# Kernel optimization log

Measured on AMD Instinct MI355X. Metric: run time of the kernel, lower is better.

The kernel has to match this reference:

```python
import jax, jax.numpy as jnp
import numpy as np

M_DIM = 1024
N_HEADS = 16
H_DIM = M_DIM // N_HEADS
FFN_H = 2 * M_DIM
B, S = 2, 2048
EPS = 1e-5
NEG = -1e9


def layernorm(x, g, b):
    mu = jnp.mean(x, axis=-1, keepdims=True)
    var = jnp.mean((x - mu) ** 2, axis=-1, keepdims=True)
    return (x - mu) * jax.lax.rsqrt(var + EPS) * g + b


def setup_inputs() -> dict:
    key = jax.random.key(0)
    ks = jax.random.split(key, 16)
    sc = 0.02
    return {
        "x": jax.random.normal(ks[0], (B, S, M_DIM), jnp.float32),
        "attention_mask": jnp.ones((B, S), jnp.int32),
        # per-head QKV projections stacked over heads: [H, M, D]
        "Wq": jax.random.normal(ks[1], (N_HEADS, M_DIM, H_DIM), jnp.float32) * sc,
        "bq": jnp.zeros((N_HEADS, H_DIM), jnp.float32),
        "Wk": jax.random.normal(ks[2], (N_HEADS, M_DIM, H_DIM), jnp.float32) * sc,
        "bk": jnp.zeros((N_HEADS, H_DIM), jnp.float32),
        "Wv": jax.random.normal(ks[3], (N_HEADS, M_DIM, H_DIM), jnp.float32) * sc,
        "bv": jnp.zeros((N_HEADS, H_DIM), jnp.float32),
        "Wo": jax.random.normal(ks[4], (M_DIM, M_DIM), jnp.float32) * sc,
        "bo": jnp.zeros((M_DIM,), jnp.float32),
        "g1": jnp.ones((M_DIM,), jnp.float32),
        "b1": jnp.zeros((M_DIM,), jnp.float32),
        "W1": jax.random.normal(ks[5], (M_DIM, FFN_H), jnp.float32) * sc,
        "bias1": jnp.zeros((FFN_H,), jnp.float32),
        "W2": jax.random.normal(ks[6], (FFN_H, M_DIM), jnp.float32) * sc,
        "bias2": jnp.zeros((M_DIM,), jnp.float32),
        "g2": jnp.ones((M_DIM,), jnp.float32),
        "b2": jnp.zeros((M_DIM,), jnp.float32),
    }


def reference(x, attention_mask, Wq, bq, Wk, bk, Wv, bv, Wo, bo, g1, b1, W1, bias1, W2, bias2, g2, b2):
    # All heads at once (the torch code loops over heads; same math).
    q = jnp.einsum("bsm,hmd->bhsd", x, Wq) + bq[None, :, None, :]
    k = jnp.einsum("bsm,hmd->bhsd", x, Wk) + bk[None, :, None, :]
    v = jnp.einsum("bsm,hmd->bhsd", x, Wv) + bv[None, :, None, :]
    scores = jnp.einsum("bhqd,bhkd->bhqk", q, k) / jnp.sqrt(jnp.float32(H_DIM))
    mask = attention_mask[:, None, None, :].astype(bool)  # [B,1,1,S] over keys
    scores = jnp.where(mask, scores, NEG)
    attn = jax.nn.softmax(scores, axis=-1)
    ctx = jnp.einsum("bhqk,bhkd->bhqd", attn, v)
    ctx = ctx.transpose(0, 2, 1, 3).reshape(x.shape[0], x.shape[1], M_DIM)  # concat heads
    out = ctx @ Wo + bo
    out = layernorm(out + x, g1, b1)
    fout = jax.nn.relu(out @ W1 + bias1) @ W2 + bias2
    out = layernorm(out + fout, g2, b2)
    return out
```

## Files before the change

kernel.cpp:

```cpp
#include <hip/hip_runtime.h>

#define MDIM 1024
#define FFH  2048
#define SEQ  2048
#define AST  72
#define VST  136
#define QSCL 0.18033688f

#if __has_builtin(__builtin_amdgcn_exp2f)
  #define EXP2(x) __builtin_amdgcn_exp2f(x)
#else
  #define EXP2(x) exp2f(x)
#endif

typedef __attribute__((ext_vector_type(8))) __bf16 bf16x8;
typedef __attribute__((ext_vector_type(4))) float floatx4;
typedef __attribute__((address_space(3))) unsigned int lds_uint;
typedef const __attribute__((address_space(1))) unsigned int g_uint;

__device__ __forceinline__ unsigned short f2bf(float f){
  union { float f; unsigned u; } v; v.f = f;
  unsigned u = v.u;
  u += 0x7fffu + ((u >> 16) & 1u);
  return (unsigned short)(u >> 16);
}
__device__ __forceinline__ unsigned short f2bf_tr(float f){
  union { float f; unsigned u; } v; v.f = f;
  return (unsigned short)(v.u >> 16);
}

__global__ void k_cvt_qb(const float* __restrict__ x, unsigned short* __restrict__ xb,
                         const float* __restrict__ bq, const float* __restrict__ bk,
                         const float* __restrict__ bv, float* __restrict__ qbias){
  const int bid = blockIdx.x, t = threadIdx.x;
  if (bid < 4096){
    int i = (bid * 256 + t) * 4;
    float4 v = *(const float4*)(x + i);
    ushort4 o;
    o.x = f2bf(v.x); o.y = f2bf(v.y); o.z = f2bf(v.z); o.w = f2bf(v.w);
    *(ushort4*)(xb + i) = o;
  } else {
    int i = (bid - 4096) * 256 + t;
    qbias[i] = (i < 1024) ? bq[i] * QSCL : (i < 2048) ? bk[i - 1024] : bv[i - 2048];
  }
}

__global__ void __launch_bounds__(256) k_prep_w(const float* __restrict__ Wo, const float* __restrict__ W1,
                                                const float* __restrict__ W2, const float* __restrict__ Wq,
                                                const float* __restrict__ Wk, const float* __restrict__ Wv,
                                                unsigned short* __restrict__ wot, unsigned short* __restrict__ w1t,
                                                unsigned short* __restrict__ w2t, unsigned short* __restrict__ wqkvt){
  __shared__ unsigned short Ts[32 * 36];
  const int t = threadIdx.x, bid = blockIdx.x;
  const int lr = t >> 3, lc4 = (t & 7) << 2;
  if (bid >= 5120){
    const int id = bid - 5120;
    const int xm = id & 31, yd = (id >> 5) & 1, z = id >> 6;
    const int tensor = z >> 4, h = z & 15;
    const float* W = (tensor == 0) ? Wq : (tensor == 1) ? Wk : Wv;
    const float scl = (tensor == 0) ? QSCL : 1.0f;
    const int m0 = xm << 5, d0 = yd << 5;
    float4 v = *(const float4*)(W + ((size_t)h << 16) + (size_t)(m0 + lr) * 64 + d0 + lc4);
    ushort4 o; o.x = f2bf(v.x * scl); o.y = f2bf(v.y * scl); o.z = f2bf(v.z * scl); o.w = f2bf(v.w * scl);
    *(ushort4*)&Ts[lr * 36 + lc4] = o;
    __syncthreads();
    ushort4 w;
    w.x = Ts[(lc4 + 0) * 36 + lr];
    w.y = Ts[(lc4 + 1) * 36 + lr];
    w.z = Ts[(lc4 + 2) * 36 + lr];
    w.w = Ts[(lc4 + 3) * 36 + lr];
    const int n = (tensor << 10) + (h << 6) + d0 + lr;
    *(ushort4*)(wqkvt + ((size_t)n << 10) + m0 + lc4) = w;
    return;
  }
  const float* src; unsigned short* dst; int K, N, k0, n0;
  if (bid < 1024){
    src = Wo; dst = wot; K = 1024; N = 1024;
    n0 = (bid & 31) << 5; k0 = (bid >> 5) << 5;
  } else if (bid < 3072){
    const int id = bid - 1024;
    src = W1; dst = w1t; K = 1024; N = 2048;
    n0 = (id & 63) << 5; k0 = (id >> 6) << 5;
  } else {
    const int id = bid - 3072;
    src = W2; dst = w2t; K = 2048; N = 1024;
    n0 = (id & 31) << 5; k0 = (id >> 5) << 5;
  }
  float4 v = *(const float4*)(src + (size_t)(k0 + lr) * N + n0 + lc4);
  ushort4 o; o.x = f2bf(v.x); o.y = f2bf(v.y); o.z = f2bf(v.z); o.w = f2bf(v.w);
  *(ushort4*)&Ts[lr * 36 + lc4] = o;
  __syncthreads();
  ushort4 w;
  w.x = Ts[(lc4 + 0) * 36 + lr];
  w.y = Ts[(lc4 + 1) * 36 + lr];
  w.z = Ts[(lc4 + 2) * 36 + lr];
  w.w = Ts[(lc4 + 3) * 36 + lr];
  *(ushort4*)(dst + (size_t)(n0 + lr) * K + k0 + lc4) = w;
}

template<int RELU, int OUTBF>
__global__ void __launch_bounds__(256) k_gemm128(const unsigned short* __restrict__ A,
                                                 const unsigned short* __restrict__ Bt,
                                                 const float* __restrict__ bias,
                                                 void* __restrict__ Cout, int N, int K){
  __shared__ unsigned short As[2 * 128 * 32];
  __shared__ unsigned short Bs[2 * 128 * 32];
  const int t = threadIdx.x;
  const int m0 = blockIdx.y << 7, n0 = blockIdx.x << 7;
  const int lane = t & 63, w = t >> 6;
  const int quad = lane >> 4, l16 = lane & 15;
  const int mw = (w & 1) << 6, nw = (w >> 1) << 6;
  floatx4 acc[4][4];
  #pragma unroll
  for (int i = 0; i < 4; i++)
    #pragma unroll
    for (int j = 0; j < 4; j++) acc[i][j] = (floatx4){0.f, 0.f, 0.f, 0.f};
  const unsigned short* Ag  = A  + (size_t)(m0 + (t >> 2)) * K + ((t & 3) << 3);
  const unsigned short* Ag2 = Ag + (size_t)64 * K;
  const unsigned short* Bg  = Bt + (size_t)(n0 + (t >> 2)) * K + ((t & 3) << 3);
  const unsigned short* Bg2 = Bg + (size_t)64 * K;
  for (int kb = 0; kb < K; kb += 64){
    #pragma unroll
    for (int s = 0; s < 2; s++){
      const int ko = kb + (s << 5), lo = (s << 12) + (t << 3);
      __builtin_amdgcn_global_load_lds((g_uint*)(Ag  + ko), (lds_uint*)&As[lo],        16, 0, 0);
      __builtin_amdgcn_global_load_lds((g_uint*)(Ag2 + ko), (lds_uint*)&As[lo + 2048], 16, 0, 0);
      __builtin_amdgcn_global_load_lds((g_uint*)(Bg  + ko), (lds_uint*)&Bs[lo],        16, 0, 0);
      __builtin_amdgcn_global_load_lds((g_uint*)(Bg2 + ko), (lds_uint*)&Bs[lo + 2048], 16, 0, 0);
    }
    __syncthreads();
    #pragma unroll
    for (int s = 0; s < 2; s++){
      const int sb = s << 12;
      bf16x8 af[4], bf[4];
      #pragma unroll
      for (int mt = 0; mt < 4; mt++)
        af[mt] = *(const bf16x8*)&As[sb + ((mw + (mt << 4) + l16) << 5) + (quad << 3)];
      #pragma unroll
      for (int nt = 0; nt < 4; nt++)
        bf[nt] = *(const bf16x8*)&Bs[sb + ((nw + (nt << 4) + l16) << 5) + (quad << 3)];
      #pragma unroll
      for (int mt = 0; mt < 4; mt++)
        #pragma unroll
        for (int nt = 0; nt < 4; nt++)
          acc[mt][nt] = __builtin_amdgcn_mfma_f32_16x16x32_bf16(af[mt], bf[nt], acc[mt][nt], 0, 0, 0);
    }
    __syncthreads();
  }
  #pragma unroll
  for (int nt = 0; nt < 4; nt++){
    const int col = n0 + nw + (nt << 4) + l16;
    const float bsv = bias[col];
    #pragma unroll
    for (int mt = 0; mt < 4; mt++){
      const int row = m0 + mw + (mt << 4) + (quad << 2);
      #pragma unroll
      for (int r = 0; r < 4; r++){
        float v = acc[mt][nt][r] + bsv;
        if (RELU) v = fmaxf(v, 0.f);
        if (OUTBF) ((unsigned short*)Cout)[(size_t)(row + r) * N + col] = f2bf(v);
        else       ((float*)Cout)[(size_t)(row + r) * N + col] = v;
      }
    }
  }
}

template<int RELU, int OUTBF>
__global__ void __launch_bounds__(256) k_gemm64n(const unsigned short* __restrict__ A,
                                                 const unsigned short* __restrict__ Bt,
                                                 const float* __restrict__ bias,
                                                 void* __restrict__ Cout, int N, int K){
  __shared__ unsigned short As[2 * 128 * 32];
  __shared__ unsigned short Bs[2 * 64 * 32];
  const int t = threadIdx.x;
  const int m0 = blockIdx.y << 7, n0 = blockIdx.x << 6;
  const int lane = t & 63, w = t >> 6;
  const int quad = lane >> 4, l16 = lane & 15;
  const int mw = (w & 1) << 6, nw = (w >> 1) << 5;
  floatx4 acc[4][2];
  #pragma unroll
  for (int i = 0; i < 4; i++)
    #pragma unroll
    for (int j = 0; j < 2; j++) acc[i][j] = (floatx4){0.f, 0.f, 0.f, 0.f};
  const unsigned short* Ag  = A  + (size_t)(m0 + (t >> 2)) * K + ((t & 3) << 3);
  const unsigned short* Ag2 = Ag + (size_t)64 * K;
  const unsigned short* Bg  = Bt + (size_t)(n0 + (t >> 2)) * K + ((t & 3) << 3);
  for (int kb = 0; kb < K; kb += 64){
    #pragma unroll
    for (int s = 0; s < 2; s++){
      const int ko = kb + (s << 5);
      __builtin_amdgcn_global_load_lds((g_uint*)(Ag  + ko), (lds_uint*)&As[(s << 12) + (t << 3)],        16, 0, 0);
      __builtin_amdgcn_global_load_lds((g_uint*)(Ag2 + ko), (lds_uint*)&As[(s << 12) + (t << 3) + 2048], 16, 0, 0);
      __builtin_amdgcn_global_load_lds((g_uint*)(Bg  + ko), (lds_uint*)&Bs[(s << 11) + (t << 3)],        16, 0, 0);
    }
    __syncthreads();
    #pragma unroll
    for (int s = 0; s < 2; s++){
      bf16x8 af[4], bf[2];
      #pragma unroll
      for (int mt = 0; mt < 4; mt++)
        af[mt] = *(const bf16x8*)&As[(s << 12) + ((mw + (mt << 4) + l16) << 5) + (quad << 3)];
      #pragma unroll
      for (int nt = 0; nt < 2; nt++)
        bf[nt] = *(const bf16x8*)&Bs[(s << 11) + ((nw + (nt << 4) + l16) << 5) + (quad << 3)];
      #pragma unroll
      for (int mt = 0; mt < 4; mt++)
        #pragma unroll
        for (int nt = 0; nt < 2; nt++)
          acc[mt][nt] = __builtin_amdgcn_mfma_f32_16x16x32_bf16(af[mt], bf[nt], acc[mt][nt], 0, 0, 0);
    }
    __syncthreads();
  }
  #pragma unroll
  for (int nt = 0; nt < 2; nt++){
    const int col = n0 + nw + (nt << 4) + l16;
    const float bsv = bias[col];
    #pragma unroll
    for (int mt = 0; mt < 4; mt++){
      const int row = m0 + mw + (mt << 4) + (quad << 2);
      #pragma unroll
      for (int r = 0; r < 4; r++){
        float v = acc[mt][nt][r] + bsv;
        if (RELU) v = fmaxf(v, 0.f);
        if (OUTBF) ((unsigned short*)Cout)[(size_t)(row + r) * N + col] = f2bf(v);
        else       ((float*)Cout)[(size_t)(row + r) * N + col] = v;
      }
    }
  }
}

__global__ void __launch_bounds__(256, 2) k_attn(const unsigned short* __restrict__ qkvb,
                                                 const int* __restrict__ amask,
                                                 unsigned short* __restrict__ ctxb){
  __shared__ __align__(16) unsigned short Ks[128 * AST];
  __shared__ __align__(16) unsigned short Vt[64 * VST];
  __shared__ __align__(16) unsigned short PQs[128 * VST];
  __shared__ int msk[128];
  const int t = threadIdx.x;
  const int w = t >> 6, lane = t & 63;
  const int quad = lane >> 4, l16 = lane & 15;
  const int b = blockIdx.y >> 4, h = blockIdx.y & 15;
  const int q0 = blockIdx.x << 7;
  const int r0 = (w << 5) + l16;
  const int r1 = r0 + 16;
  const int sr = t >> 2, sc = (t & 3) << 4;
  const int kg = t >> 4, dc = (t & 15) << 2;

  {
    const unsigned short* qs = qkvb + (size_t)((b << 11) + q0 + (t >> 1)) * 3072 + (h << 6) + ((t & 1) << 5);
    unsigned short* qd = &PQs[(t >> 1) * VST + ((t & 1) << 5)];
    *(uint4*)(qd)      = *(const uint4*)(qs);
    *(uint4*)(qd + 8)  = *(const uint4*)(qs + 8);
    *(uint4*)(qd + 16) = *(const uint4*)(qs + 16);
    *(uint4*)(qd + 24) = *(const uint4*)(qs + 24);
  }
  __syncthreads();
  const bf16x8 qa0 = *(const bf16x8*)&PQs[r0 * VST + (quad << 3)];
  const bf16x8 qa1 = *(const bf16x8*)&PQs[r0 * VST + (quad << 3) + 32];
  const bf16x8 qb0 = *(const bf16x8*)&PQs[r1 * VST + (quad << 3)];
  const bf16x8 qb1 = *(const bf16x8*)&PQs[r1 * VST + (quad << 3) + 32];

  floatx4 accA[4], accB[4];
  #pragma unroll
  for (int i = 0; i < 4; i++){
    accA[i] = (floatx4){0.f, 0.f, 0.f, 0.f};
    accB[i] = (floatx4){0.f, 0.f, 0.f, 0.f};
  }
  float l_runA = 0.f, l_runB = 0.f;

  const unsigned short* kbase  = qkvb + (size_t)((b << 11) + sr) * 3072 + 1024 + (h << 6) + sc;
  const unsigned short* kbase2 = kbase + (size_t)64 * 3072;
  const unsigned short* vbase  = qkvb + (size_t)((b << 11) + (kg << 2)) * 3072 + 2048 + (h << 6) + dc;
  const unsigned short* vbase2 = vbase + (size_t)64 * 3072;
  const int* mbase = amask + (b << 11);

  uint4 krA, krB, krC, krD;
  ushort4 va0, va1, va2, va3, vb0, vb1, vb2, vb3;
  int mreg = 1;
  {
    krA = *(const uint4*)kbase;
    krB = *(const uint4*)(kbase + 8);
    krC = *(const uint4*)kbase2;
    krD = *(const uint4*)(kbase2 + 8);
    va0 = *(const ushort4*)(vbase);
    va1 = *(const ushort4*)(vbase + 3072);
    va2 = *(const ushort4*)(vbase + 2 * 3072);
    va3 = *(const ushort4*)(vbase + 3 * 3072);
    vb0 = *(const ushort4*)(vbase2);
    vb1 = *(const ushort4*)(vbase2 + 3072);
    vb2 = *(const ushort4*)(vbase2 + 2 * 3072);
    vb3 = *(const ushort4*)(vbase2 + 3 * 3072);
    if (t < 128) mreg = mbase[t];
  }

  for (int k0 = 0; k0 < SEQ; k0 += 128){
    __syncthreads();
    *(uint4*)&Ks[sr * AST + sc]            = krA;
    *(uint4*)&Ks[sr * AST + sc + 8]        = krB;
    *(uint4*)&Ks[(sr + 64) * AST + sc]     = krC;
    *(uint4*)&Ks[(sr + 64) * AST + sc + 8] = krD;
    {
      ushort4 c;
      c.x = va0.x; c.y = va1.x; c.z = va2.x; c.w = va3.x; *(ushort4*)&Vt[(dc + 0) * VST + (kg << 2)] = c;
      c.x = va0.y; c.y = va1.y; c.z = va2.y; c.w = va3.y; *(ushort4*)&Vt[(dc + 1) * VST + (kg << 2)] = c;
      c.x = va0.z; c.y = va1.z; c.z = va2.z; c.w = va3.z; *(ushort4*)&Vt[(dc + 2) * VST + (kg << 2)] = c;
      c.x = va0.w; c.y = va1.w; c.z = va2.w; c.w = va3.w; *(ushort4*)&Vt[(dc + 3) * VST + (kg << 2)] = c;
      c.x = vb0.x; c.y = vb1.x; c.z = vb2.x; c.w = vb3.x; *(ushort4*)&Vt[(dc + 0) * VST + ((kg + 16) << 2)] = c;
      c.x = vb0.y; c.y = vb1.y; c.z = vb2.y; c.w = vb3.y; *(ushort4*)&Vt[(dc + 1) * VST + ((kg + 16) << 2)] = c;
      c.x = vb0.z; c.y = vb1.z; c.z = vb2.z; c.w = vb3.z; *(ushort4*)&Vt[(dc + 2) * VST + ((kg + 16) << 2)] = c;
      c.x = vb0.w; c.y = vb1.w; c.z = vb2.w; c.w = vb3.w; *(ushort4*)&Vt[(dc + 3) * VST + ((kg + 16) << 2)] = c;
    }
    if (t < 128) msk[t] = mreg;
    __syncthreads();
    if (k0 + 128 < SEQ){
      const unsigned short* ks  = kbase  + (size_t)(k0 + 128) * 3072;
      const unsigned short* ks2 = kbase2 + (size_t)(k0 + 128) * 3072;
      krA = *(const uint4*)ks;
      krB = *(const uint4*)(ks + 8);
      krC = *(const uint4*)ks2;
      krD = *(const uint4*)(ks2 + 8);
      const unsigned short* vs  = vbase  + (size_t)(k0 + 128) * 3072;
      const unsigned short* vs2 = vbase2 + (size_t)(k0 + 128) * 3072;
      va0 = *(const ushort4*)(vs);
      va1 = *(const ushort4*)(vs + 3072);
      va2 = *(const ushort4*)(vs + 2 * 3072);
      va3 = *(const ushort4*)(vs + 3 * 3072);
      vb0 = *(const ushort4*)(vs2);
      vb1 = *(const ushort4*)(vs2 + 3072);
      vb2 = *(const ushort4*)(vs2 + 2 * 3072);
      vb3 = *(const ushort4*)(vs2 + 3 * 3072);
      if (t < 128) mreg = mbase[k0 + 128 + t];
    }

    float lsA = 0.f, lsB = 0.f;
    #pragma unroll
    for (int mt = 0; mt < 8; mt++){
      const unsigned short* kp = &Ks[((mt << 4) + l16) * AST + (quad << 3)];
      const bf16x8 kf0 = *(const bf16x8*)(kp);
      const bf16x8 kf1 = *(const bf16x8*)(kp + 32);
      floatx4 sA = (floatx4){0.f, 0.f, 0.f, 0.f};
      floatx4 sB = (floatx4){0.f, 0.f, 0.f, 0.f};
      __builtin_amdgcn_s_setprio(1);
      sA = __builtin_amdgcn_mfma_f32_16x16x32_bf16(kf0, qa0, sA, 0, 0, 0);
      sA = __builtin_amdgcn_mfma_f32_16x16x32_bf16(kf1, qa1, sA, 0, 0, 0);
      sB = __builtin_amdgcn_mfma_f32_16x16x32_bf16(kf0, qb0, sB, 0, 0, 0);
      sB = __builtin_amdgcn_mfma_f32_16x16x32_bf16(kf1, qb1, sB, 0, 0, 0);
      __builtin_amdgcn_s_setprio(0);
      const int4 m4 = *(const int4*)&msk[(mt << 4) + (quad << 2)];
      float pA0 = m4.x ? EXP2(sA[0]) : 0.f;
      float pA1 = m4.y ? EXP2(sA[1]) : 0.f;
      float pA2 = m4.z ? EXP2(sA[2]) : 0.f;
      float pA3 = m4.w ? EXP2(sA[3]) : 0.f;
      lsA += pA0 + pA1 + pA2 + pA3;
      ushort4 oA;
      oA.x = f2bf_tr(pA0); oA.y = f2bf_tr(pA1); oA.z = f2bf_tr(pA2); oA.w = f2bf_tr(pA3);
      *(ushort4*)&PQs[r0 * VST + (mt << 4) + (quad << 2)] = oA;
      float pB0 = m4.x ? EXP2(sB[0]) : 0.f;
      float pB1 = m4.y ? EXP2(sB[1]) : 0.f;
      float pB2 = m4.z ? EXP2(sB[2]) : 0.f;
      float pB3 = m4.w ? EXP2(sB[3]) : 0.f;
      lsB += pB0 + pB1 + pB2 + pB3;
      ushort4 oB;
      oB.x = f2bf_tr(pB0); oB.y = f2bf_tr(pB1); oB.z = f2bf_tr(pB2); oB.w = f2bf_tr(pB3);
      *(ushort4*)&PQs[r1 * VST + (mt << 4) + (quad << 2)] = oB;
    }
    lsA += __shfl_xor(lsA, 16);
    lsA += __shfl_xor(lsA, 32);
    l_runA += lsA;
    lsB += __shfl_xor(lsB, 16);
    lsB += __shfl_xor(lsB, 32);
    l_runB += lsB;
    asm volatile("" ::: "memory");
    bf16x8 pA[4], pB[4];
    #pragma unroll
    for (int s = 0; s < 4; s++){
      pA[s] = *(const bf16x8*)&PQs[r0 * VST + (s << 5) + (quad << 3)];
      pB[s] = *(const bf16x8*)&PQs[r1 * VST + (s << 5) + (quad << 3)];
    }
    #pragma unroll
    for (int mt = 0; mt < 4; mt++){
      const unsigned short* vp = &Vt[((mt << 4) + l16) * VST + (quad << 3)];
      __builtin_amdgcn_s_setprio(1);
      #pragma unroll
      for (int s = 0; s < 4; s++){
        const bf16x8 vf = *(const bf16x8*)(vp + (s << 5));
        accA[mt] = __builtin_amdgcn_mfma_f32_16x16x32_bf16(vf, pA[s], accA[mt], 0, 0, 0);
        accB[mt] = __builtin_amdgcn_mfma_f32_16x16x32_bf16(vf, pB[s], accB[mt], 0, 0, 0);
      }
      __builtin_amdgcn_s_setprio(0);
    }
  }
  const float liA = 1.f / l_runA;
  const float liB = 1.f / l_runB;
  unsigned short* oA = ctxb + (size_t)((b << 11) + q0 + r0) * 1024 + (h << 6);
  unsigned short* oB = ctxb + (size_t)((b << 11) + q0 + r1) * 1024 + (h << 6);
  #pragma unroll
  for (int mt = 0; mt < 4; mt++){
    ushort4 o;
    o.x = f2bf(accA[mt][0] * liA);
    o.y = f2bf(accA[mt][1] * liA);
    o.z = f2bf(accA[mt][2] * liA);
    o.w = f2bf(accA[mt][3] * liA);
    *(ushort4*)&oA[(mt << 4) + (quad << 2)] = o;
    o.x = f2bf(accB[mt][0] * liB);
    o.y = f2bf(accB[mt][1] * liB);
    o.z = f2bf(accB[mt][2] * liB);
    o.w = f2bf(accB[mt][3] * liB);
    *(ushort4*)&oB[(mt << 4) + (quad << 2)] = o;
  }
}

__global__ void __launch_bounds__(256) k_ln(const unsigned short* __restrict__ a,
                                            const float* __restrict__ res,
                                            const float* __restrict__ gg, const float* __restrict__ bb,
                                            float* __restrict__ out, unsigned short* __restrict__ outb){
  const int row = blockIdx.x, t = threadIdx.x;
  const ushort4 au = ((const ushort4*)(a + (size_t)row * 1024))[t];
  const float4 rv = ((const float4*)(res + (size_t)row * 1024))[t];
  float4 v;
  { union { unsigned u; float f; } c;
    c.u = (unsigned)au.x << 16; v.x = c.f + rv.x;
    c.u = (unsigned)au.y << 16; v.y = c.f + rv.y;
    c.u = (unsigned)au.z << 16; v.z = c.f + rv.z;
    c.u = (unsigned)au.w << 16; v.w = c.f + rv.w; }
  float sum = v.x + v.y + v.z + v.w;
  float ss  = v.x * v.x + v.y * v.y + v.z * v.z + v.w * v.w;
  #pragma unroll
  for (int off = 32; off > 0; off >>= 1){
    sum += __shfl_down(sum, off);
    ss  += __shfl_down(ss, off);
  }
  __shared__ float red[8];
  const int w = t >> 6;
  if ((t & 63) == 0){ red[w] = sum; red[4 + w] = ss; }
  __syncthreads();
  const float S  = red[0] + red[1] + red[2] + red[3];
  const float SS = red[4] + red[5] + red[6] + red[7];
  const float mu  = S * (1.f / 1024.f);
  const float var = SS * (1.f / 1024.f) - mu * mu;
  const float rs  = rsqrtf(var + 1e-5f);
  const float4 gv = ((const float4*)gg)[t];
  const float4 bv = ((const float4*)bb)[t];
  float4 o;
  o.x = (v.x - mu) * rs * gv.x + bv.x;
  o.y = (v.y - mu) * rs * gv.y + bv.y;
  o.z = (v.z - mu) * rs * gv.z + bv.z;
  o.w = (v.w - mu) * rs * gv.w + bv.w;
  ((float4*)(out + (size_t)row * 1024))[t] = o;
  if (outb){
    ushort4 ob; ob.x = f2bf(o.x); ob.y = f2bf(o.y); ob.z = f2bf(o.z); ob.w = f2bf(o.w);
    ((ushort4*)(outb + (size_t)row * 1024))[t] = ob;
  }
}

extern "C" void kernel_launch(void* const* d_in, const int* in_sizes, int n_in,
                              void* d_out, int out_size, void* d_ws, size_t ws_size,
                              hipStream_t stream){
  const float* x     = (const float*)d_in[0];
  const int*   amask = (const int*)d_in[1];
  const float* Wq    = (const float*)d_in[2];
  const float* bq    = (const float*)d_in[3];
  const float* Wk    = (const float*)d_in[4];
  const float* bk    = (const float*)d_in[5];
  const float* Wv    = (const float*)d_in[6];
  const float* bv    = (const float*)d_in[7];
  const float* Wo    = (const float*)d_in[8];
  const float* bo    = (const float*)d_in[9];
  const float* g1    = (const float*)d_in[10];
  const float* b1    = (const float*)d_in[11];
  const float* W1    = (const float*)d_in[12];
  const float* bias1 = (const float*)d_in[13];
  const float* W2    = (const float*)d_in[14];
  const float* bias2 = (const float*)d_in[15];
  const float* g2    = (const float*)d_in[16];
  const float* b2    = (const float*)d_in[17];

  char* ws = (char*)d_ws;
  unsigned short* xb    = (unsigned short*)(ws + 0);
  unsigned short* wqkvt = (unsigned short*)(ws + 8388608);
  float*          qbias = (float*)         (ws + 14680064);
  unsigned short* wot   = (unsigned short*)(ws + 14692352);
  unsigned short* w1t   = (unsigned short*)(ws + 16789504);
  unsigned short* w2t   = (unsigned short*)(ws + 20983808);
  unsigned short* ctxb  = (unsigned short*)(ws + 25178112);
  unsigned short* attnb = (unsigned short*)(ws + 33566720);
  unsigned short* fbufb = attnb;
  unsigned short* qkvb  = (unsigned short*)(ws + 50343936);
  float*          out1  = (float*)         (ws + 50343936);
  unsigned short* out1b = (unsigned short*)(ws + 50343936 + 25165824);
  unsigned short* h1    = (unsigned short*)(ws + 50343936 + 33554432);

  k_cvt_qb<<<dim3(4108), dim3(256), 0, stream>>>(x, xb, bq, bk, bv, qbias);
  k_prep_w<<<dim3(8192), dim3(256), 0, stream>>>(Wo, W1, W2, Wq, Wk, Wv, wot, w1t, w2t, wqkvt);

  k_gemm128<0,1><<<dim3(24, 32), dim3(256), 0, stream>>>(xb, wqkvt, qbias, qkvb, 3072, 1024);
  k_attn<<<dim3(16, 32), dim3(256), 0, stream>>>(qkvb, amask, ctxb);
  k_gemm64n<0,1><<<dim3(16, 32), dim3(256), 0, stream>>>(ctxb, wot, bo, attnb, MDIM, 1024);
  k_ln<<<dim3(4096), dim3(256), 0, stream>>>(attnb, x, g1, b1, out1, out1b);
  k_gemm128<1,1><<<dim3(16, 32), dim3(256), 0, stream>>>(out1b, w1t, bias1, h1, FFH, 1024);
  k_gemm64n<0,1><<<dim3(16, 32), dim3(256), 0, stream>>>(h1, w2t, bias2, fbufb, MDIM, 2048);
  k_ln<<<dim3(4096), dim3(256), 0, stream>>>(fbufb, out1, g2, b2, (float*)d_out, nullptr);
}
```

Measured before the change: 327.8 us.

## Double-buffer K/V in LDS and keep softmax probabilities in registers for PV MFMA

```diff
diff --git a/kernel.cpp b/kernel.cpp
--- a/kernel.cpp
+++ b/kernel.cpp
@@ -15,6 +15,7 @@
 
 typedef __attribute__((ext_vector_type(8))) __bf16 bf16x8;
 typedef __attribute__((ext_vector_type(4))) float floatx4;
+typedef __attribute__((ext_vector_type(8))) unsigned short ushort8;
 typedef __attribute__((address_space(3))) unsigned int lds_uint;
 typedef const __attribute__((address_space(1))) unsigned int g_uint;
 
@@ -232,10 +233,9 @@
 __global__ void __launch_bounds__(256, 2) k_attn(const unsigned short* __restrict__ qkvb,
                                                  const int* __restrict__ amask,
                                                  unsigned short* __restrict__ ctxb){
-  __shared__ __align__(16) unsigned short Ks[128 * AST];
-  __shared__ __align__(16) unsigned short Vt[64 * VST];
-  __shared__ __align__(16) unsigned short PQs[128 * VST];
-  __shared__ int msk[128];
+  __shared__ __align__(16) unsigned short Ks[2][128 * AST];
+  __shared__ __align__(16) unsigned short Vt[2][64 * VST];
+  __shared__ __align__(16) int msk[2][128];
   const int t = threadIdx.x;
   const int w = t >> 6, lane = t & 63;
   const int quad = lane >> 4, l16 = lane & 15;
@@ -245,20 +245,23 @@
   const int r1 = r0 + 16;
   const int sr = t >> 2, sc = (t & 3) << 4;
   const int kg = t >> 4, dc = (t & 15) << 2;
+  const int swz  = (dc >> 4) & 3;
+  const int pc0  = ((((kg & 3) | ((kg >> 3) << 2)) ^ swz) << 3) | (((kg >> 2) & 1) << 2);
 
   {
-    const unsigned short* qs = qkvb + (size_t)((b << 11) + q0 + (t >> 1)) * 3072 + (h << 6) + ((t & 1) << 5);
-    unsigned short* qd = &PQs[(t >> 1) * VST + ((t & 1) << 5)];
+    const int qr = t >> 1, qc = (t & 1) << 5;
+    const unsigned short* qs = qkvb + (size_t)((b << 11) + q0 + qr) * 3072 + (h << 6) + qc;
+    unsigned short* qd = &Ks[0][qr * AST + qc];
     *(uint4*)(qd)      = *(const uint4*)(qs);
     *(uint4*)(qd + 8)  = *(const uint4*)(qs + 8);
     *(uint4*)(qd + 16) = *(const uint4*)(qs + 16);
     *(uint4*)(qd + 24) = *(const uint4*)(qs + 24);
   }
   __syncthreads();
-  const bf16x8 qa0 = *(const bf16x8*)&PQs[r0 * VST + (quad << 3)];
-  const bf16x8 qa1 = *(const bf16x8*)&PQs[r0 * VST + (quad << 3) + 32];
-  const bf16x8 qb0 = *(const bf16x8*)&PQs[r1 * VST + (quad << 3)];
-  const bf16x8 qb1 = *(const bf16x8*)&PQs[r1 * VST + (quad << 3) + 32];
+  const bf16x8 qa0 = *(const bf16x8*)&Ks[0][r0 * AST + (quad << 3)];
+  const bf16x8 qa1 = *(const bf16x8*)&Ks[0][r0 * AST + (quad << 3) + 32];
+  const bf16x8 qb0 = *(const bf16x8*)&Ks[0][r1 * AST + (quad << 3)];
+  const bf16x8 qb1 = *(const bf16x8*)&Ks[0][r1 * AST + (quad << 3) + 32];
 
   floatx4 accA[4], accB[4];
   #pragma unroll
@@ -277,119 +280,128 @@
   uint4 krA, krB, krC, krD;
   ushort4 va0, va1, va2, va3, vb0, vb1, vb2, vb3;
   int mreg = 1;
-  {
-    krA = *(const uint4*)kbase;
-    krB = *(const uint4*)(kbase + 8);
-    krC = *(const uint4*)kbase2;
-    krD = *(const uint4*)(kbase2 + 8);
-    va0 = *(const ushort4*)(vbase);
-    va1 = *(const ushort4*)(vbase + 3072);
-    va2 = *(const ushort4*)(vbase + 2 * 3072);
-    va3 = *(const ushort4*)(vbase + 3 * 3072);
-    vb0 = *(const ushort4*)(vbase2);
-    vb1 = *(const ushort4*)(vbase2 + 3072);
-    vb2 = *(const ushort4*)(vbase2 + 2 * 3072);
-    vb3 = *(const ushort4*)(vbase2 + 3 * 3072);
-    if (t < 128) mreg = mbase[t];
-  }
-
-  for (int k0 = 0; k0 < SEQ; k0 += 128){
+
+#define LOADT(tt) { \
+    const size_t off = (size_t)((tt) << 7) * 3072; \
+    krA = *(const uint4*)(kbase + off); \
+    krB = *(const uint4*)(kbase + off + 8); \
+    krC = *(const uint4*)(kbase2 + off); \
+    krD = *(const uint4*)(kbase2 + off + 8); \
+    va0 = *(const ushort4*)(vbase + off); \
+    va1 = *(const ushort4*)(vbase + off + 3072); \
+    va2 = *(const ushort4*)(vbase + off + 2 * 3072); \
+    va3 = *(const ushort4*)(vbase + off + 3 * 3072); \
+    vb0 = *(const ushort4*)(vbase2 + off); \
+    vb1 = *(const ushort4*)(vbase2 + off + 3072); \
+    vb2 = *(const ushort4*)(vbase2 + off + 2 * 3072); \
+    vb3 = *(const ushort4*)(vbase2 + off + 3 * 3072); \
+    if (t < 128) mreg = mbase[((tt) << 7) + t]; \
+  }
+
+#define STORET(dst) { \
+    unsigned short* Kd = Ks[dst]; \
+    unsigned short* Vd = Vt[dst]; \
+    *(uint4*)&Kd[sr * AST + sc]            = krA; \
+    *(uint4*)&Kd[sr * AST + sc + 8]        = krB; \
+    *(uint4*)&Kd[(sr + 64) * AST + sc]     = krC; \
+    *(uint4*)&Kd[(sr + 64) * AST + sc + 8] = krD; \
+    ushort4 cc; \
+    cc.x = va0.x; cc.y = va1.x; cc.z = va2.x; cc.w = va3.x; *(ushort4*)&Vd[(dc + 0) * VST + pc0] = cc; \
+    cc.x = va0.y; cc.y = va1.y; cc.z = va2.y; cc.w = va3.y; *(ushort4*)&Vd[(dc + 1) * VST + pc0] = cc; \
+    cc.x = va0.z; cc.y = va1.z; cc.z = va2.z; cc.w = va3.z; *(ushort4*)&Vd[(dc + 2) * VST + pc0] = cc; \
+    cc.x = va0.w; cc.y = va1.w; cc.z = va2.w; cc.w = va3.w; *(ushort4*)&Vd[(dc + 3) * VST + pc0] = cc; \
+    cc.x = vb0.x; cc.y = vb1.x; cc.z = vb2.x; cc.w = vb3.x; *(ushort4*)&Vd[(dc + 0) * VST + pc0 + 64] = cc; \
+    cc.x = vb0.y; cc.y = vb1.y; cc.z = vb2.y; cc.w = vb3.y; *(ushort4*)&Vd[(dc + 1) * VST + pc0 + 64] = cc; \
+    cc.x = vb0.z; cc.y = vb1.z; cc.z = vb2.z; cc.w = vb3.z; *(ushort4*)&Vd[(dc + 2) * VST + pc0 + 64] = cc; \
+    cc.x = vb0.w; cc.y = vb1.w; cc.z = vb2.w; cc.w = vb3.w; *(ushort4*)&Vd[(dc + 3) * VST + pc0 + 64] = cc; \
+    if (t < 128) msk[dst][t] = mreg; \
+  }
+
+  LOADT(0);
+  __syncthreads();
+  STORET(0);
+  LOADT(1);
+  __syncthreads();
+
+  int c = 0;
+  for (int kt = 0; kt < 16; kt++){
+    if (kt + 1 < 16) STORET(c ^ 1);
+    if (kt + 2 < 16) LOADT(kt + 2);
+    {
+      const unsigned short* Kc = Ks[c];
+      const unsigned short* Vc = Vt[c];
+      const int* Mc = msk[c];
+      float lsA = 0.f, lsB = 0.f;
+      #pragma unroll
+      for (int s = 0; s < 4; s++){
+        const unsigned short* kp = &Kc[((s << 5) + l16) * AST + (quad << 3)];
+        const bf16x8 k00 = *(const bf16x8*)(kp);
+        const bf16x8 k01 = *(const bf16x8*)(kp + 32);
+        const bf16x8 k10 = *(const bf16x8*)(kp + (AST << 4));
+        const bf16x8 k11 = *(const bf16x8*)(kp + (AST << 4) + 32);
+        floatx4 sA0 = (floatx4){0.f, 0.f, 0.f, 0.f};
+        floatx4 sB0 = (floatx4){0.f, 0.f, 0.f, 0.f};
+        floatx4 sA1 = (floatx4){0.f, 0.f, 0.f, 0.f};
+        floatx4 sB1 = (floatx4){0.f, 0.f, 0.f, 0.f};
+        __builtin_amdgcn_s_setprio(1);
+        sA0 = __builtin_amdgcn_mfma_f32_16x16x32_bf16(k00, qa0, sA0, 0, 0, 0);
+        sA0 = __builtin_amdgcn_mfma_f32_16x16x32_bf16(k01, qa1, sA0, 0, 0, 0);
+        sB0 = __builtin_amdgcn_mfma_f32_16x16x32_bf16(k00, qb0, sB0, 0, 0, 0);
+        sB0 = __builtin_amdgcn_mfma_f32_16x16x32_bf16(k01, qb1, sB0, 0, 0, 0);
+        sA1 = __builtin_amdgcn_mfma_f32_16x16x32_bf16(k10, qa0, sA1, 0, 0, 0);
+        sA1 = __builtin_amdgcn_mfma_f32_16x16x32_bf16(k11, qa1, sA1, 0, 0, 0);
+        sB1 = __builtin_amdgcn_mfma_f32_16x16x32_bf16(k10, qb0, sB1, 0, 0, 0);
+        sB1 = __builtin_amdgcn_mfma_f32_16x16x32_bf16(k11, qb1, sB1, 0, 0, 0);
+        __builtin_amdgcn_s_setprio(0);
+        const int4 m0 = *(const int4*)&Mc[(s << 5) + (quad << 2)];
+        const int4 m1 = *(const int4*)&Mc[(s << 5) + 16 + (quad << 2)];
+        const float a0 = m0.x ? EXP2(sA0[0]) : 0.f;
+        const float a1 = m0.y ? EXP2(sA0[1]) : 0.f;
+        const float a2 = m0.z ? EXP2(sA0[2]) : 0.f;
+        const float a3 = m0.w ? EXP2(sA0[3]) : 0.f;
+        const float a4 = m1.x ? EXP2(sA1[0]) : 0.f;
+        const float a5 = m1.y ? EXP2(sA1[1]) : 0.f;
+        const float a6 = m1.z ? EXP2(sA1[2]) : 0.f;
+        const float a7 = m1.w ? EXP2(sA1[3]) : 0.f;
+        const float b0 = m0.x ? EXP2(sB0[0]) : 0.f;
+        const float b1 = m0.y ? EXP2(sB0[1]) : 0.f;
+        const float b2 = m0.z ? EXP2(sB0[2]) : 0.f;
+        const float b3 = m0.w ? EXP2(sB0[3]) : 0.f;
+        const float b4 = m1.x ? EXP2(sB1[0]) : 0.f;
+        const float b5 = m1.y ? EXP2(sB1[1]) : 0.f;
+        const float b6 = m1.z ? EXP2(sB1[2]) : 0.f;
+        const float b7 = m1.w ? EXP2(sB1[3]) : 0.f;
+        lsA += (a0 + a1) + (a2 + a3) + (a4 + a5) + (a6 + a7);
+        lsB += (b0 + b1) + (b2 + b3) + (b4 + b5) + (b6 + b7);
+        ushort8 uA, uB;
+        uA[0] = f2bf_tr(a0); uA[1] = f2bf_tr(a1); uA[2] = f2bf_tr(a2); uA[3] = f2bf_tr(a3);
+        uA[4] = f2bf_tr(a4); uA[5] = f2bf_tr(a5); uA[6] = f2bf_tr(a6); uA[7] = f2bf_tr(a7);
+        uB[0] = f2bf_tr(b0); uB[1] = f2bf_tr(b1); uB[2] = f2bf_tr(b2); uB[3] = f2bf_tr(b3);
+        uB[4] = f2bf_tr(b4); uB[5] = f2bf_tr(b5); uB[6] = f2bf_tr(b6); uB[7] = f2bf_tr(b7);
+        const bf16x8 pfA = __builtin_bit_cast(bf16x8, uA);
+        const bf16x8 pfB = __builtin_bit_cast(bf16x8, uB);
+        __builtin_amdgcn_s_setprio(1);
+        #pragma unroll
+        for (int mt = 0; mt < 4; mt++){
+          const bf16x8 vf = *(const bf16x8*)&Vc[((mt << 4) + l16) * VST + ((((s << 2) + quad) ^ mt) << 3)];
+          accA[mt] = __builtin_amdgcn_mfma_f32_16x16x32_bf16(vf, pfA, accA[mt], 0, 0, 0);
+          accB[mt] = __builtin_amdgcn_mfma_f32_16x16x32_bf16(vf, pfB, accB[mt], 0, 0, 0);
+        }
+        __builtin_amdgcn_s_setprio(0);
+      }
+      l_runA += lsA;
+      l_runB += lsB;
+    }
     __syncthreads();
-    *(uint4*)&Ks[sr * AST + sc]            = krA;
-    *(uint4*)&Ks[sr * AST + sc + 8]        = krB;
-    *(uint4*)&Ks[(sr + 64) * AST + sc]     = krC;
-    *(uint4*)&Ks[(sr + 64) * AST + sc + 8] = krD;
-    {
-      ushort4 c;
-      c.x = va0.x; c.y = va1.x; c.z = va2.x; c.w = va3.x; *(ushort4*)&Vt[(dc + 0) * VST + (kg << 2)] = c;
-      c.x = va0.y; c.y = va1.y; c.z = va2.y; c.w = va3.y; *(ushort4*)&Vt[(dc + 1) * VST + (kg << 2)] = c;
-      c.x = va0.z; c.y = va1.z; c.z = va2.z; c.w = va3.z; *(ushort4*)&Vt[(dc + 2) * VST + (kg << 2)] = c;
-      c.x = va0.w; c.y = va1.w; c.z = va2.w; c.w = va3.w; *(ushort4*)&Vt[(dc + 3) * VST + (kg << 2)] = c;
-      c.x = vb0.x; c.y = vb1.x; c.z = vb2.x; c.w = vb3.x; *(ushort4*)&Vt[(dc + 0) * VST + ((kg + 16) << 2)] = c;
-      c.x = vb0.y; c.y = vb1.y; c.z = vb2.y; c.w = vb3.y; *(ushort4*)&Vt[(dc + 1) * VST + ((kg + 16) << 2)] = c;
-      c.x = vb0.z; c.y = vb1.z; c.z = vb2.z; c.w = vb3.z; *(ushort4*)&Vt[(dc + 2) * VST + ((kg + 16) << 2)] = c;
-      c.x = vb0.w; c.y = vb1.w; c.z = vb2.w; c.w = vb3.w; *(ushort4*)&Vt[(dc + 3) * VST + ((kg + 16) << 2)] = c;
-    }
-    if (t < 128) msk[t] = mreg;
-    __syncthreads();
-    if (k0 + 128 < SEQ){
-      const unsigned short* ks  = kbase  + (size_t)(k0 + 128) * 3072;
-      const unsigned short* ks2 = kbase2 + (size_t)(k0 + 128) * 3072;
-      krA = *(const uint4*)ks;
-      krB = *(const uint4*)(ks + 8);
-      krC = *(const uint4*)ks2;
-      krD = *(const uint4*)(ks2 + 8);
-      const unsigned short* vs  = vbase  + (size_t)(k0 + 128) * 3072;
-      const unsigned short* vs2 = vbase2 + (size_t)(k0 + 128) * 3072;
-      va0 = *(const ushort4*)(vs);
-      va1 = *(const ushort4*)(vs + 3072);
-      va2 = *(const ushort4*)(vs + 2 * 3072);
-      va3 = *(const ushort4*)(vs + 3 * 3072);
-      vb0 = *(const ushort4*)(vs2);
-      vb1 = *(const ushort4*)(vs2 + 3072);
-      vb2 = *(const ushort4*)(vs2 + 2 * 3072);
-      vb3 = *(const ushort4*)(vs2 + 3 * 3072);
-      if (t < 128) mreg = mbase[k0 + 128 + t];
-    }
-
-    float lsA = 0.f, lsB = 0.f;
-    #pragma unroll
-    for (int mt = 0; mt < 8; mt++){
-      const unsigned short* kp = &Ks[((mt << 4) + l16) * AST + (quad << 3)];
-      const bf16x8 kf0 = *(const bf16x8*)(kp);
-      const bf16x8 kf1 = *(const bf16x8*)(kp + 32);
-      floatx4 sA = (floatx4){0.f, 0.f, 0.f, 0.f};
-      floatx4 sB = (floatx4){0.f, 0.f, 0.f, 0.f};
-      __builtin_amdgcn_s_setprio(1);
-      sA = __builtin_amdgcn_mfma_f32_16x16x32_bf16(kf0, qa0, sA, 0, 0, 0);
-      sA = __builtin_amdgcn_mfma_f32_16x16x32_bf16(kf1, qa1, sA, 0, 0, 0);
-      sB = __builtin_amdgcn_mfma_f32_16x16x32_bf16(kf0, qb0, sB, 0, 0, 0);
-      sB = __builtin_amdgcn_mfma_f32_16x16x32_bf16(kf1, qb1, sB, 0, 0, 0);
-      __builtin_amdgcn_s_setprio(0);
-      const int4 m4 = *(const int4*)&msk[(mt << 4) + (quad << 2)];
-      float pA0 = m4.x ? EXP2(sA[0]) : 0.f;
-      float pA1 = m4.y ? EXP2(sA[1]) : 0.f;
-      float pA2 = m4.z ? EXP2(sA[2]) : 0.f;
-      float pA3 = m4.w ? EXP2(sA[3]) : 0.f;
-      lsA += pA0 + pA1 + pA2 + pA3;
-      ushort4 oA;
-      oA.x = f2bf_tr(pA0); oA.y = f2bf_tr(pA1); oA.z = f2bf_tr(pA2); oA.w = f2bf_tr(pA3);
-      *(ushort4*)&PQs[r0 * VST + (mt << 4) + (quad << 2)] = oA;
-      float pB0 = m4.x ? EXP2(sB[0]) : 0.f;
-      float pB1 = m4.y ? EXP2(sB[1]) : 0.f;
-      float pB2 = m4.z ? EXP2(sB[2]) : 0.f;
-      float pB3 = m4.w ? EXP2(sB[3]) : 0.f;
-      lsB += pB0 + pB1 + pB2 + pB3;
-      ushort4 oB;
-      oB.x = f2bf_tr(pB0); oB.y = f2bf_tr(pB1); oB.z = f2bf_tr(pB2); oB.w = f2bf_tr(pB3);
-      *(ushort4*)&PQs[r1 * VST + (mt << 4) + (quad << 2)] = oB;
-    }
-    lsA += __shfl_xor(lsA, 16);
-    lsA += __shfl_xor(lsA, 32);
-    l_runA += lsA;
-    lsB += __shfl_xor(lsB, 16);
-    lsB += __shfl_xor(lsB, 32);
-    l_runB += lsB;
-    asm volatile("" ::: "memory");
-    bf16x8 pA[4], pB[4];
-    #pragma unroll
-    for (int s = 0; s < 4; s++){
-      pA[s] = *(const bf16x8*)&PQs[r0 * VST + (s << 5) + (quad << 3)];
-      pB[s] = *(const bf16x8*)&PQs[r1 * VST + (s << 5) + (quad << 3)];
-    }
-    #pragma unroll
-    for (int mt = 0; mt < 4; mt++){
-      const unsigned short* vp = &Vt[((mt << 4) + l16) * VST + (quad << 3)];
-      __builtin_amdgcn_s_setprio(1);
-      #pragma unroll
-      for (int s = 0; s < 4; s++){
-        const bf16x8 vf = *(const bf16x8*)(vp + (s << 5));
-        accA[mt] = __builtin_amdgcn_mfma_f32_16x16x32_bf16(vf, pA[s], accA[mt], 0, 0, 0);
-        accB[mt] = __builtin_amdgcn_mfma_f32_16x16x32_bf16(vf, pB[s], accB[mt], 0, 0, 0);
-      }
-      __builtin_amdgcn_s_setprio(0);
-    }
-  }
+    c ^= 1;
+  }
+#undef LOADT
+#undef STORET
+
+  l_runA += __shfl_xor(l_runA, 16);
+  l_runA += __shfl_xor(l_runA, 32);
+  l_runB += __shfl_xor(l_runB, 16);
+  l_runB += __shfl_xor(l_runB, 32);
   const float liA = 1.f / l_runA;
   const float liB = 1.f / l_runB;
   unsigned short* oA = ctxb + (size_t)((b << 11) + q0 + r0) * 1024 + (h << 6);
```

Result: faster. 312.6 us (-4.6%).
